# Performance work log

Hardware: AMD Instinct MI355X
Metric: run time of the kernel (lower is better)

## Reference

```python
import jax, jax.numpy as jnp
import numpy as np

N_NODES = 100000
N_EDGES = 3200000
NFEAT, NHID, NOUT = 256, 128, 64


def spmm(edge_row, edge_col, edge_val, dense):
    # out[r] = sum_{e: row[e]==r} val[e] * dense[col[e]]
    gathered = dense[edge_col] * edge_val[:, None]  # [E, F]
    return jax.ops.segment_sum(gathered, edge_row, num_segments=N_NODES)


def setup_inputs() -> dict:
    key = jax.random.key(0)
    ks = jax.random.split(key, 8)
    stdv1 = 1.0 / np.sqrt(NHID)
    stdv2 = 1.0 / np.sqrt(NOUT)
    return {
        "x": jax.random.normal(ks[0], (N_NODES, NFEAT), dtype=jnp.float32),
        "edge_row": jax.random.randint(ks[1], (N_EDGES,), 0, N_NODES, dtype=jnp.int32),
        "edge_col": jax.random.randint(ks[2], (N_EDGES,), 0, N_NODES, dtype=jnp.int32),
        "edge_val": jax.random.uniform(ks[3], (N_EDGES,), dtype=jnp.float32),
        "W1": jax.random.uniform(ks[4], (NFEAT, NHID), jnp.float32, -stdv1, stdv1),
        "b1": jax.random.uniform(ks[5], (NHID,), jnp.float32, -stdv1, stdv1),
        "W2": jax.random.uniform(ks[6], (NHID, NOUT), jnp.float32, -stdv2, stdv2),
        "b2": jax.random.uniform(ks[7], (NOUT,), jnp.float32, -stdv2, stdv2),
    }


def reference(x, edge_row, edge_col, edge_val, W1, b1, W2, b2):
    # layer 1: dense projection, SpMM aggregate, bias, ReLU
    support = x @ W1                                   # [N, NHID]
    h = spmm(edge_row, edge_col, edge_val, support) + b1
    h = jax.nn.relu(h)
    # dropout skipped (eval mode: training=False)
    # layer 2
    support2 = h @ W2                                  # [N, NOUT]
    out = spmm(edge_row, edge_col, edge_val, support2) + b2
    return out
```

## Files before the change

kernel.cpp:

```cpp
#include <hip/hip_runtime.h>
#include <hip/hip_bf16.h>

#define N_NODES 100000
#define N_EDGES 3200000
#define NFEAT 256
#define NHID 128
#define NOUT 64

#define BSHIFT 8
#define BROWS 256
#define NBUCK 391
#define EPB 4096
#define NBLK1 ((N_EDGES + EPB - 1) / EPB)

#define CSHIFT 12
#define NCLS 32

#define SM_SC    0
#define SM_SB    32768
#define SM_HIST  40960
#define SM_DELTA 42524
#define SM_SCANT 44088
#define SM_BYTES 44160

typedef __attribute__((ext_vector_type(8))) short short8;
typedef __attribute__((ext_vector_type(8))) unsigned short ushort8_t;
typedef __attribute__((ext_vector_type(4))) float f32x4;

__device__ __forceinline__ unsigned short f2bf(float f) {
    union { float f; unsigned int u; } v; v.f = f;
    unsigned int r = v.u + 0x7fffu + ((v.u >> 16) & 1u);
    return (unsigned short)(r >> 16);
}
__device__ __forceinline__ float bflo(unsigned int u) { return __uint_as_float(u << 16); }
__device__ __forceinline__ float bfhi(unsigned int u) { return __uint_as_float(u & 0xffff0000u); }


__global__ __launch_bounds__(256) void bcount_cvtw(const int* __restrict__ erow,
                                                   int* __restrict__ Mt,
                                                   const float* __restrict__ W1,
                                                   const float* __restrict__ W2,
                                                   unsigned short* __restrict__ W1b,
                                                   unsigned short* __restrict__ W2b) {
    __shared__ int h[NBUCK];
    if (blockIdx.x >= NBLK1) {
        const int i = (blockIdx.x - NBLK1) * 256 + threadIdx.x;
        if (i < NFEAT * NHID) W1b[i] = f2bf(W1[i]);
        if (i < NHID * NOUT)  W2b[i] = f2bf(W2[i]);
        return;
    }
    for (int i = threadIdx.x; i < NBUCK; i += 256) h[i] = 0;
    __syncthreads();
    const int base = blockIdx.x * EPB;
    const int n = min(EPB, N_EDGES - base);
    for (int i = threadIdx.x; i < n; i += 256)
        atomicAdd(&h[erow[base + i] >> BSHIFT], 1);
    __syncthreads();
    for (int b = threadIdx.x; b < NBUCK; b += 256)
        Mt[(size_t)b * NBLK1 + blockIdx.x] = h[b];
}


__global__ __launch_bounds__(256) void colscan_kernel(int* __restrict__ Mt,
                                                      int* __restrict__ btot) {
    const int wv = threadIdx.x >> 6, lane = threadIdx.x & 63;
    const int b = blockIdx.x * 4 + wv;
    if (b >= NBUCK) return;
    int* row = Mt + (size_t)b * NBLK1;
    int carry = 0;
    for (int t = 0; t < NBLK1; t += 64) {
        int i = t + lane;
        int v = (i < NBLK1) ? row[i] : 0;
        int x = v;
        #pragma unroll
        for (int off = 1; off < 64; off <<= 1) {
            int tt = __shfl_up(x, off);
            if (lane >= off) x += tt;
        }
        if (i < NBLK1) row[i] = carry + x - v;
        carry += __shfl(x, 63);
    }
    if (lane == 0) btot[b] = carry;
}


__global__ __launch_bounds__(1024) void bscan_kernel(const int* __restrict__ btot,
                                                     int* __restrict__ bbase) {
    __shared__ int wsum[16];
    const int tid = threadIdx.x;
    const int lane = tid & 63;
    int v = (tid < NBUCK) ? btot[tid] : 0;
    int x = v;
    #pragma unroll
    for (int off = 1; off < 64; off <<= 1) {
        int t = __shfl_up(x, off);
        if (lane >= off) x += t;
    }
    if (lane == 63) wsum[tid >> 6] = x;
    __syncthreads();
    if (tid < 16) {
        int s = wsum[tid];
        #pragma unroll
        for (int off = 1; off < 16; off <<= 1) {
            int t = __shfl_up(s, off);
            if (tid >= off) s += t;
        }
        wsum[tid] = s;
    }
    __syncthreads();
    if (tid >= 64) x += wsum[(tid >> 6) - 1];
    if (tid < NBUCK) bbase[tid] = x - v;
    if (tid == NBUCK - 1) bbase[NBUCK] = x;
}


__device__ __forceinline__ void binsort_role(int blk, char* sm,
                                             const int* __restrict__ erow,
                                             const int* __restrict__ ecol,
                                             const float* __restrict__ eval,
                                             const int* __restrict__ Mt,
                                             const int* __restrict__ btot,
                                             const int* __restrict__ bbase,
                                             int2* __restrict__ tmp) {
    int2* sc = (int2*)(sm + SM_SC);
    unsigned short* sb = (unsigned short*)(sm + SM_SB);
    int* hist  = (int*)(sm + SM_HIST);
    int* delta = (int*)(sm + SM_DELTA);
    int* scan_t = (int*)(sm + SM_SCANT);

    const int tid = threadIdx.x;
    const int base = blk * EPB;
    const int n = min(EPB, N_EDGES - base);

    int v0 = 0, v1 = 0, v2 = 0, v3 = 0;
    int m0 = 0, m1 = 0, m2 = 0, m3 = 0;
    {
        const int i0 = tid * 4;
        #define LOADCNT(k, vk, mk) { \
            int idx = i0 + k; \
            if (idx < NBUCK) { \
                mk = Mt[(size_t)idx * NBLK1 + blk]; \
                int nx = (blk + 1 < NBLK1) ? Mt[(size_t)idx * NBLK1 + blk + 1] : btot[idx]; \
                vk = nx - mk; \
            } }
        LOADCNT(0, v0, m0) LOADCNT(1, v1, m1) LOADCNT(2, v2, m2) LOADCNT(3, v3, m3)
        #undef LOADCNT
    }
    int s4 = v0 + v1 + v2 + v3;
    int xi = s4;
    const int lane = tid & 63;
    #pragma unroll
    for (int off = 1; off < 64; off <<= 1) {
        int t = __shfl_up(xi, off);
        if (lane >= off) xi += t;
    }
    if (lane == 63) scan_t[tid >> 6] = xi;
    __syncthreads();
    if (tid == 0) {
        int run = 0;
        #pragma unroll
        for (int w = 0; w < 4; ++w) { int t = scan_t[w]; scan_t[w] = run; run += t; }
    }
    __syncthreads();
    {
        int e0 = scan_t[tid >> 6] + xi - s4;
        int i0 = tid * 4;
        int ex[4] = {e0, e0 + v0, e0 + v0 + v1, e0 + v0 + v1 + v2};
        int mm[4] = {m0, m1, m2, m3};
        #pragma unroll
        for (int k = 0; k < 4; ++k) {
            int idx = i0 + k;
            if (idx < NBUCK) {
                hist[idx] = ex[k];
                delta[idx] = bbase[idx] + mm[k] - ex[k];
            }
        }
    }
    __syncthreads();

    for (int i = tid; i < n; i += 256) {
        int r = erow[base + i];
        int b = r >> BSHIFT;
        int rl = r & (BROWS - 1);
        int pos = atomicAdd(&hist[b], 1);
        sc[pos] = make_int2((rl << 17) | ecol[base + i], __float_as_int(eval[base + i]));
        sb[pos] = (unsigned short)b;
    }
    __syncthreads();

    for (int i = tid; i < n; i += 256) {
        int b = sb[i];
        tmp[delta[b] + i] = sc[i];
    }
}

__device__ __forceinline__ void gemm1_role(int bid, char* sm,
                                           const float* __restrict__ X,
                                           const unsigned short* __restrict__ Wb,
                                           unsigned short* __restrict__ Y) {
    unsigned short* bt = (unsigned short*)sm;
    const int tid = threadIdx.x;
    const int lane = tid & 63;
    const int w = tid >> 6;
    const int rb = bid * 128 + w * 32;
    const int lr = lane & 15;
    const int kg = lane >> 4;
    const int M = N_NODES;

    f32x4 acc[2][8];
    #pragma unroll
    for (int a = 0; a < 2; ++a)
        #pragma unroll
        for (int nf = 0; nf < 8; ++nf)
            #pragma unroll
            for (int i = 0; i < 4; ++i) acc[a][nf][i] = 0.f;

    for (int ph = 0; ph < 2; ++ph) {
        if (ph) __syncthreads();
        {
            const int nn = tid & 127;
            const int kb = tid >> 7;
            #pragma unroll
            for (int kk0 = 0; kk0 < 64; kk0 += 8) {
                const int kk = kb * 64 + kk0;
                unsigned short p[8];
                #pragma unroll
                for (int i = 0; i < 8; ++i)
                    p[i] = Wb[(size_t)(ph * 128 + kk + i) * NHID + nn];
                unsigned int byte = (unsigned int)nn * 256 + (unsigned int)kk * 2;
                byte ^= (unsigned int)(nn & 7) << 4;
                *(ushort8_t*)((char*)bt + byte) = *(const ushort8_t*)p;
            }
        }
        __syncthreads();

        #pragma unroll
        for (int ks = 0; ks < 4; ++ks) {
            const int k0 = ph * 128 + ks * 32 + kg * 8;
            short8 a0, a1;
            #pragma unroll
            for (int af = 0; af < 2; ++af) {
                const int row = rb + af * 16 + lr;
                short8 r;
                if (row < M) {
                    const float* p = X + (size_t)row * NFEAT + k0;
                    float4 u0 = *(const float4*)p;
                    float4 u1 = *(const float4*)(p + 4);
                    unsigned short q[8] = {f2bf(u0.x), f2bf(u0.y), f2bf(u0.z), f2bf(u0.w),
                                           f2bf(u1.x), f2bf(u1.y), f2bf(u1.z), f2bf(u1.w)};
                    r = *(const short8*)q;
                } else {
                    #pragma unroll
                    for (int i = 0; i < 8; ++i) r[i] = 0;
                }
                if (af == 0) a0 = r; else a1 = r;
            }
            #pragma unroll
            for (int nf = 0; nf < 8; ++nf) {
                const int nn = nf * 16 + lr;
                unsigned int byte = (unsigned int)nn * 256 + (unsigned int)(ks * 32 + kg * 8) * 2;
                byte ^= (unsigned int)(nn & 7) << 4;
                short8 bfr = *(const short8*)((const char*)bt + byte);
                acc[0][nf] = __builtin_amdgcn_mfma_f32_16x16x32_bf16(a0, bfr, acc[0][nf], 0, 0, 0);
                acc[1][nf] = __builtin_amdgcn_mfma_f32_16x16x32_bf16(a1, bfr, acc[1][nf], 0, 0, 0);
            }
        }
    }

    #pragma unroll
    for (int af = 0; af < 2; ++af)
        #pragma unroll
        for (int nf = 0; nf < 8; ++nf)
            #pragma unroll
            for (int i = 0; i < 4; ++i) {
                const int r = rb + af * 16 + kg * 4 + i;
                if (r < M) Y[(size_t)r * NHID + nf * 16 + lr] = f2bf(acc[af][nf][i]);
            }
}

__global__ __launch_bounds__(256) void fused_bg(const int* __restrict__ erow,
                                                const int* __restrict__ ecol,
                                                const float* __restrict__ eval,
                                                const int* __restrict__ Mt,
                                                const int* __restrict__ btot,
                                                const int* __restrict__ bbase,
                                                int2* __restrict__ tmp,
                                                const float* __restrict__ X,
                                                const unsigned short* __restrict__ W1b,
                                                unsigned short* __restrict__ Y) {
    extern __shared__ char sm[];
    const int idx = blockIdx.x >> 1;
    if (blockIdx.x & 1) gemm1_role(idx, sm, X, W1b, Y);
    else                binsort_role(idx, sm, erow, ecol, eval, Mt, btot, bbase, tmp);
}


__global__ __launch_bounds__(256) void rowsort_kernel(const int* __restrict__ bbase,
                                                      const int2* __restrict__ tmp,
                                                      int2* __restrict__ ec2,
                                                      int* __restrict__ rowptr) {
    __shared__ int h[BROWS * NCLS];
    __shared__ int wq[4];

    const int b = blockIdx.x;
    const int s = bbase[b], e = bbase[b + 1];
    const int n = e - s;
    const int tid = threadIdx.x;
    const int lane = tid & 63;

    for (int k = tid; k < BROWS * NCLS; k += 256) h[k] = 0;
    __syncthreads();

    for (int i = tid; i < n; i += 256) {
        unsigned int xx = (unsigned)tmp[s + i].x;
        unsigned int rl = xx >> 17;
        unsigned int c  = (xx & 0x1FFFFu) >> CSHIFT;
        atomicAdd(&h[(rl << 5) | ((c + rl) & 31)], 1);
    }
    __syncthreads();

    int tot = 0;
    #pragma unroll
    for (int j = 0; j < NCLS; ++j) tot += h[(tid << 5) | ((j + tid) & 31)];

    int x = tot;
    #pragma unroll
    for (int off = 1; off < 64; off <<= 1) {
        int t = __shfl_up(x, off);
        if (lane >= off) x += t;
    }
    if (lane == 63) wq[tid >> 6] = x;
    __syncthreads();
    if (tid == 0) {
        int run = 0;
        #pragma unroll
        for (int w = 0; w < 4; ++w) { int t = wq[w]; wq[w] = run; run += t; }
    }
    __syncthreads();
    x += wq[tid >> 6];
    {
        const int grow = b * BROWS + tid;
        if (grow < N_NODES) rowptr[grow + 1] = s + x;
        if (b == 0 && tid == 0) rowptr[0] = 0;
    }
    {
        int run = s + (x - tot);
        #pragma unroll
        for (int j = 0; j < NCLS; ++j) {
            const int idx = (tid << 5) | ((j + tid) & 31);
            const int cnt = h[idx];
            h[idx] = run;
            run += cnt;
        }
    }
    __syncthreads();

    for (int i = tid; i < n; i += 256) {
        int2 d = tmp[s + i];
        unsigned int xx = (unsigned)d.x;
        unsigned int rl = xx >> 17;
        unsigned int c  = (xx & 0x1FFFFu) >> CSHIFT;
        int pos = atomicAdd(&h[(rl << 5) | ((c + rl) & 31)], 1);
        ec2[pos] = make_int2(d.x & 0x1FFFF, d.y);
    }
}


template<int N, int K>
__global__ __launch_bounds__(256) void gemm_mfma(const unsigned short* __restrict__ X,
                                                 const unsigned short* __restrict__ Wb,
                                                 unsigned short* __restrict__ Y, int M) {
    __shared__ unsigned short bt[N * K];
    const int tid = threadIdx.x;

    {
        const int n = tid & (N - 1);
        const int kb = tid / N;
        const int kspan = K / (256 / N);
        for (int k0 = kb * kspan; k0 < (kb + 1) * kspan; k0 += 8) {
            unsigned short p[8];
            #pragma unroll
            for (int i = 0; i < 8; ++i) p[i] = Wb[(size_t)(k0 + i) * N + n];
            unsigned int byte = (unsigned int)n * (K * 2) + (unsigned int)k0 * 2;
            byte ^= (unsigned int)(n & 7) << 4;
            *(ushort8_t*)((char*)bt + byte) = *(const ushort8_t*)p;
        }
    }
    __syncthreads();

    const int lane = tid & 63;
    const int w = tid >> 6;
    const int rb = blockIdx.x * 128 + w * 32;
    const int lr = lane & 15;
    const int kg = lane >> 4;
    constexpr int NF = N / 16;
    constexpr int KS = K / 32;

    f32x4 acc[2][NF];
    #pragma unroll
    for (int a = 0; a < 2; ++a)
        #pragma unroll
        for (int nf = 0; nf < NF; ++nf)
            #pragma unroll
            for (int i = 0; i < 4; ++i) acc[a][nf][i] = 0.f;

    auto loadA = [&](int af, int ks) -> short8 {
        const int row = rb + af * 16 + lr;
        const int k0 = ks * 32 + kg * 8;
        short8 r;
        if (row < M) {
            r = *(const short8*)(X + (size_t)row * K + k0);
        } else {
            #pragma unroll
            for (int i = 0; i < 8; ++i) r[i] = 0;
        }
        return r;
    };
    auto loadB = [&](int nf, int ks) -> short8 {
        const int n = nf * 16 + lr;
        unsigned int byte = (unsigned int)n * (K * 2) + (unsigned int)(ks * 32 + kg * 8) * 2;
        byte ^= (unsigned int)(n & 7) << 4;
        return *(const short8*)((const char*)bt + byte);
    };

    #pragma unroll
    for (int ks = 0; ks < KS; ++ks) {
        short8 a0 = loadA(0, ks), a1 = loadA(1, ks);
        #pragma unroll
        for (int nf = 0; nf < NF; ++nf) {
            short8 bfr = loadB(nf, ks);
            acc[0][nf] = __builtin_amdgcn_mfma_f32_16x16x32_bf16(a0, bfr, acc[0][nf], 0, 0, 0);
            acc[1][nf] = __builtin_amdgcn_mfma_f32_16x16x32_bf16(a1, bfr, acc[1][nf], 0, 0, 0);
        }
    }

    #pragma unroll
    for (int af = 0; af < 2; ++af)
        #pragma unroll
        for (int nf = 0; nf < NF; ++nf)
            #pragma unroll
            for (int i = 0; i < 4; ++i) {
                const int r = rb + af * 16 + kg * 4 + i;
                if (r < M) Y[(size_t)r * N + nf * 16 + lr] = f2bf(acc[af][nf][i]);
            }
}


__global__ __launch_bounds__(256) void spmm1_kernel(const int* __restrict__ rp,
                                                    const int2* __restrict__ ec,
                                                    const unsigned int* __restrict__ d32,
                                                    const float* __restrict__ bias,
                                                    unsigned short* __restrict__ out) {
    const int lane = threadIdx.x & 63;
    const int row = blockIdx.x * 4 + (threadIdx.x >> 6);
    if (row >= N_NODES) return;
    const int s = __builtin_amdgcn_readfirstlane(rp[row]);
    const int e = __builtin_amdgcn_readfirstlane(rp[row + 1]);
    float a0 = 0.f, a1 = 0.f, b0 = 0.f, b1 = 0.f;
    float c0a = 0.f, c1a = 0.f, d0a = 0.f, d1a = 0.f;
    int j = s;
    for (; j + 16 <= e; j += 16) {
        int2 q0 = ec[j],      q1 = ec[j + 1],  q2 = ec[j + 2],  q3 = ec[j + 3];
        int2 q4 = ec[j + 4],  q5 = ec[j + 5],  q6 = ec[j + 6],  q7 = ec[j + 7];
        int2 q8 = ec[j + 8],  q9 = ec[j + 9],  qa = ec[j + 10], qb = ec[j + 11];
        int2 qc = ec[j + 12], qd = ec[j + 13], qe = ec[j + 14], qf = ec[j + 15];
        unsigned int u0 = d32[(size_t)q0.x * 64 + lane];
        unsigned int u1 = d32[(size_t)q1.x * 64 + lane];
        unsigned int u2 = d32[(size_t)q2.x * 64 + lane];
        unsigned int u3 = d32[(size_t)q3.x * 64 + lane];
        unsigned int u4 = d32[(size_t)q4.x * 64 + lane];
        unsigned int u5 = d32[(size_t)q5.x * 64 + lane];
        unsigned int u6 = d32[(size_t)q6.x * 64 + lane];
        unsigned int u7 = d32[(size_t)q7.x * 64 + lane];
        unsigned int u8 = d32[(size_t)q8.x * 64 + lane];
        unsigned int u9 = d32[(size_t)q9.x * 64 + lane];
        unsigned int ua = d32[(size_t)qa.x * 64 + lane];
        unsigned int ub = d32[(size_t)qb.x * 64 + lane];
        unsigned int uc = d32[(size_t)qc.x * 64 + lane];
        unsigned int ud = d32[(size_t)qd.x * 64 + lane];
        unsigned int ue = d32[(size_t)qe.x * 64 + lane];
        unsigned int uf = d32[(size_t)qf.x * 64 + lane];
        float v0 = __int_as_float(q0.y), v1 = __int_as_float(q1.y);
        float v2 = __int_as_float(q2.y), v3 = __int_as_float(q3.y);
        float v4 = __int_as_float(q4.y), v5 = __int_as_float(q5.y);
        float v6 = __int_as_float(q6.y), v7 = __int_as_float(q7.y);
        float v8 = __int_as_float(q8.y), v9 = __int_as_float(q9.y);
        float va = __int_as_float(qa.y), vb = __int_as_float(qb.y);
        float vc = __int_as_float(qc.y), vd = __int_as_float(qd.y);
        float ve = __int_as_float(qe.y), vf = __int_as_float(qf.y);
        a0 += v0 * bflo(u0); a1 += v0 * bfhi(u0);
        b0 += v1 * bflo(u1); b1 += v1 * bfhi(u1);
        c0a += v2 * bflo(u2); c1a += v2 * bfhi(u2);
        d0a += v3 * bflo(u3); d1a += v3 * bfhi(u3);
        a0 += v4 * bflo(u4); a1 += v4 * bfhi(u4);
        b0 += v5 * bflo(u5); b1 += v5 * bfhi(u5);
        c0a += v6 * bflo(u6); c1a += v6 * bfhi(u6);
        d0a += v7 * bflo(u7); d1a += v7 * bfhi(u7);
        a0 += v8 * bflo(u8); a1 += v8 * bfhi(u8);
        b0 += v9 * bflo(u9); b1 += v9 * bfhi(u9);
        c0a += va * bflo(ua); c1a += va * bfhi(ua);
        d0a += vb * bflo(ub); d1a += vb * bfhi(ub);
        a0 += vc * bflo(uc); a1 += vc * bfhi(uc);
        b0 += vd * bflo(ud); b1 += vd * bfhi(ud);
        c0a += ve * bflo(ue); c1a += ve * bfhi(ue);
        d0a += vf * bflo(uf); d1a += vf * bfhi(uf);
    }
    for (; j + 8 <= e; j += 8) {
        int2 q0 = ec[j],     q1 = ec[j + 1], q2 = ec[j + 2], q3 = ec[j + 3];
        int2 q4 = ec[j + 4], q5 = ec[j + 5], q6 = ec[j + 6], q7 = ec[j + 7];
        unsigned int u0 = d32[(size_t)q0.x * 64 + lane];
        unsigned int u1 = d32[(size_t)q1.x * 64 + lane];
        unsigned int u2 = d32[(size_t)q2.x * 64 + lane];
        unsigned int u3 = d32[(size_t)q3.x * 64 + lane];
        unsigned int u4 = d32[(size_t)q4.x * 64 + lane];
        unsigned int u5 = d32[(size_t)q5.x * 64 + lane];
        unsigned int u6 = d32[(size_t)q6.x * 64 + lane];
        unsigned int u7 = d32[(size_t)q7.x * 64 + lane];
        float v0 = __int_as_float(q0.y), v1 = __int_as_float(q1.y);
        float v2 = __int_as_float(q2.y), v3 = __int_as_float(q3.y);
        float v4 = __int_as_float(q4.y), v5 = __int_as_float(q5.y);
        float v6 = __int_as_float(q6.y), v7 = __int_as_float(q7.y);
        a0 += v0 * bflo(u0); a1 += v0 * bfhi(u0);
        b0 += v1 * bflo(u1); b1 += v1 * bfhi(u1);
        c0a += v2 * bflo(u2); c1a += v2 * bfhi(u2);
        d0a += v3 * bflo(u3); d1a += v3 * bfhi(u3);
        a0 += v4 * bflo(u4); a1 += v4 * bfhi(u4);
        b0 += v5 * bflo(u5); b1 += v5 * bfhi(u5);
        c0a += v6 * bflo(u6); c1a += v6 * bfhi(u6);
        d0a += v7 * bflo(u7); d1a += v7 * bfhi(u7);
    }
    for (; j < e; ++j) {
        int2 c = ec[j];
        float v = __int_as_float(c.y);
        unsigned int u = d32[(size_t)c.x * 64 + lane];
        a0 += v * bflo(u);
        a1 += v * bfhi(u);
    }
    a0 += b0 + c0a + d0a; a1 += b1 + c1a + d1a;
    float2 bp = *(const float2*)(bias + 2 * lane);
    float r0 = fmaxf(a0 + bp.x, 0.f);
    float r1 = fmaxf(a1 + bp.y, 0.f);
    unsigned int pack = (unsigned int)f2bf(r0) | ((unsigned int)f2bf(r1) << 16);
    *(unsigned int*)(out + (size_t)row * 128 + 2 * lane) = pack;
}


__global__ __launch_bounds__(256) void spmm2_kernel(const int* __restrict__ rp,
                                                    const int2* __restrict__ ec,
                                                    const unsigned int* __restrict__ d32,
                                                    const float* __restrict__ bias,
                                                    float* __restrict__ out) {
    const int lane = threadIdx.x & 63;
    const int row = blockIdx.x * 4 + (threadIdx.x >> 6);
    if (row >= N_NODES) return;
    const int s = __builtin_amdgcn_readfirstlane(rp[row]);
    const int e = __builtin_amdgcn_readfirstlane(rp[row + 1]);
    const int eh = lane >> 5, cl = lane & 31;
    float a0 = 0.f, a1 = 0.f, b0 = 0.f, b1 = 0.f;
    float c0a = 0.f, c1a = 0.f, d0a = 0.f, d1a = 0.f;
    int j = s;
    for (; j + 16 <= e; j += 16) {
        int2 q0 = ec[j + eh],      q1 = ec[j + 2 + eh];
        int2 q2 = ec[j + 4 + eh],  q3 = ec[j + 6 + eh];
        int2 q4 = ec[j + 8 + eh],  q5 = ec[j + 10 + eh];
        int2 q6 = ec[j + 12 + eh], q7 = ec[j + 14 + eh];
        unsigned int u0 = d32[(size_t)q0.x * 32 + cl];
        unsigned int u1 = d32[(size_t)q1.x * 32 + cl];
        unsigned int u2 = d32[(size_t)q2.x * 32 + cl];
        unsigned int u3 = d32[(size_t)q3.x * 32 + cl];
        unsigned int u4 = d32[(size_t)q4.x * 32 + cl];
        unsigned int u5 = d32[(size_t)q5.x * 32 + cl];
        unsigned int u6 = d32[(size_t)q6.x * 32 + cl];
        unsigned int u7 = d32[(size_t)q7.x * 32 + cl];
        float v0 = __int_as_float(q0.y), v1 = __int_as_float(q1.y);
        float v2 = __int_as_float(q2.y), v3 = __int_as_float(q3.y);
        float v4 = __int_as_float(q4.y), v5 = __int_as_float(q5.y);
        float v6 = __int_as_float(q6.y), v7 = __int_as_float(q7.y);
        a0 += v0 * bflo(u0); a1 += v0 * bfhi(u0);
        b0 += v1 * bflo(u1); b1 += v1 * bfhi(u1);
        c0a += v2 * bflo(u2); c1a += v2 * bfhi(u2);
        d0a += v3 * bflo(u3); d1a += v3 * bfhi(u3);
        a0 += v4 * bflo(u4); a1 += v4 * bfhi(u4);
        b0 += v5 * bflo(u5); b1 += v5 * bfhi(u5);
        c0a += v6 * bflo(u6); c1a += v6 * bfhi(u6);
        d0a += v7 * bflo(u7); d1a += v7 * bfhi(u7);
    }
    for (; j + 8 <= e; j += 8) {
        int2 q0 = ec[j + eh],     q1 = ec[j + 2 + eh];
        int2 q2 = ec[j + 4 + eh], q3 = ec[j + 6 + eh];
        unsigned int u0 = d32[(size_t)q0.x * 32 + cl];
        unsigned int u1 = d32[(size_t)q1.x * 32 + cl];
        unsigned int u2 = d32[(size_t)q2.x * 32 + cl];
        unsigned int u3 = d32[(size_t)q3.x * 32 + cl];
        float v0 = __int_as_float(q0.y), v1 = __int_as_float(q1.y);
        float v2 = __int_as_float(q2.y), v3 = __int_as_float(q3.y);
        a0 += v0 * bflo(u0); a1 += v0 * bfhi(u0);
        b0 += v1 * bflo(u1); b1 += v1 * bfhi(u1);
        c0a += v2 * bflo(u2); c1a += v2 * bfhi(u2);
        d0a += v3 * bflo(u3); d1a += v3 * bfhi(u3);
    }
    for (; j < e; j += 2) {
        const int j2 = j + eh;
        if (j2 < e) {
            int2 cv = ec[j2];
            float v = __int_as_float(cv.y);
            unsigned int u = d32[(size_t)cv.x * 32 + cl];
            a0 += v * bflo(u);
            a1 += v * bfhi(u);
        }
    }
    a0 += b0 + c0a + d0a; a1 += b1 + c1a + d1a;
    a0 += __shfl_xor(a0, 32);
    a1 += __shfl_xor(a1, 32);
    if (eh == 0) {
        float2 bp = *(const float2*)(bias + 2 * cl);
        *(float2*)(out + (size_t)row * 64 + 2 * cl) = make_float2(a0 + bp.x, a1 + bp.y);
    }
}


extern "C" void kernel_launch(void* const* d_in, const int* in_sizes, int n_in,
                              void* d_out, int out_size, void* d_ws, size_t ws_size,
                              hipStream_t stream) {
    const float* x    = (const float*)d_in[0];
    const int*   erow = (const int*)d_in[1];
    const int*   ecol = (const int*)d_in[2];
    const float* evalv = (const float*)d_in[3];
    const float* W1   = (const float*)d_in[4];
    const float* b1   = (const float*)d_in[5];
    const float* W2   = (const float*)d_in[6];
    const float* b2   = (const float*)d_in[7];
    float* out = (float*)d_out;

    char* wsp = (char*)d_ws;
    size_t off = 0;
    auto alloc = [&](size_t bytes) -> void* {
        void* p = wsp + off;
        off = (off + bytes + 255) & ~(size_t)255;
        return p;
    };
    unsigned short* support = (unsigned short*)alloc((size_t)N_NODES * NHID * 2);
    unsigned short* hbuf    = (unsigned short*)alloc((size_t)N_NODES * NHID * 2);
    int2*  tmp     = (int2*)alloc((size_t)N_EDGES * 8);
    int2*  ec2     = (int2*)alloc((size_t)N_EDGES * 8);
    int*   Mt      = (int*)alloc((size_t)NBUCK * NBLK1 * 4);
    int*   btot    = (int*)alloc((size_t)NBUCK * 4);
    int*   bbase   = (int*)alloc((size_t)(NBUCK + 1) * 4);
    int*   rowptr  = (int*)alloc((size_t)(N_NODES + 1) * 4);
    unsigned short* W1b = (unsigned short*)alloc((size_t)NFEAT * NHID * 2);
    unsigned short* W2b = (unsigned short*)alloc((size_t)NHID * NOUT * 2);

    bcount_cvtw<<<NBLK1 + 128, 256, 0, stream>>>(erow, Mt, W1, W2, W1b, W2b);
    colscan_kernel<<<(NBUCK + 3) / 4, 256, 0, stream>>>(Mt, btot);
    bscan_kernel<<<1, 1024, 0, stream>>>(btot, bbase);
    fused_bg<<<2 * NBLK1, 256, SM_BYTES, stream>>>(erow, ecol, evalv, Mt, btot, bbase,
                                                   tmp, x, W1b, support);
    rowsort_kernel<<<NBUCK, 256, 0, stream>>>(bbase, tmp, ec2, rowptr);

    spmm1_kernel<<<(N_NODES + 3) / 4, 256, 0, stream>>>(rowptr, ec2, (const unsigned int*)support, b1, hbuf);
    gemm_mfma<NOUT, NHID><<<(N_NODES + 127) / 128, 256, 0, stream>>>(hbuf, W2b, support, N_NODES);
    spmm2_kernel<<<(N_NODES + 3) / 4, 256, 0, stream>>>(rowptr, ec2, (const unsigned int*)support, b2, out);
}
```

Before: 331.3 us.

## Column-chunk SpMM traversal with multi-row waves for dense-row cache locality

Rowsort now emits per-row offsets for each of 13 column chunks (chunk width 8192 columns) in a new rowptr2 array. Both SpMM kernels give each wave 25 rows and walk all of them chunk by chunk, keeping 25 pairs of accumulators in registers. The aim is to keep the gathered dense rows within a small column band at any moment so they stay resident in L2. The cost is far fewer waves, very short inner loops per chunk (about two or three edges), heavy register use, and extra rowptr2 traffic, all of which can reduce the memory-level parallelism that a gather-bound kernel relies on.

```diff
diff --git a/kernel.cpp b/kernel.cpp
--- a/kernel.cpp
+++ b/kernel.cpp
@@ -13,8 +13,10 @@
 #define EPB 4096
 #define NBLK1 ((N_EDGES + EPB - 1) / EPB)
 
-#define CSHIFT 12
-#define NCLS 32
+#define CSHIFT 13
+#define NCLS 16
+#define NCHUNK 13
+#define RPW 25
 
 #define SM_SC    0
 #define SM_SB    32768
@@ -298,7 +300,8 @@
 __global__ __launch_bounds__(256) void rowsort_kernel(const int* __restrict__ bbase,
                                                       const int2* __restrict__ tmp,
                                                       int2* __restrict__ ec2,
-                                                      int* __restrict__ rowptr) {
+                                                      int* __restrict__ rowptr,
+                                                      int* __restrict__ rowptr2) {
     __shared__ int h[BROWS * NCLS];
     __shared__ int wq[4];
 
@@ -315,13 +318,13 @@
         unsigned int xx = (unsigned)tmp[s + i].x;
         unsigned int rl = xx >> 17;
         unsigned int c  = (xx & 0x1FFFFu) >> CSHIFT;
-        atomicAdd(&h[(rl << 5) | ((c + rl) & 31)], 1);
+        atomicAdd(&h[(rl << 4) | ((c + rl) & 15)], 1);
     }
     __syncthreads();
 
     int tot = 0;
     #pragma unroll
-    for (int j = 0; j < NCLS; ++j) tot += h[(tid << 5) | ((j + tid) & 31)];
+    for (int j = 0; j < NCLS; ++j) tot += h[(tid << 4) | ((j + tid) & 15)];
 
     int x = tot;
     #pragma unroll
@@ -338,18 +341,18 @@
     }
     __syncthreads();
     x += wq[tid >> 6];
-    {
-        const int grow = b * BROWS + tid;
-        if (grow < N_NODES) rowptr[grow + 1] = s + x;
-        if (b == 0 && tid == 0) rowptr[0] = 0;
-    }
+    const int grow = b * BROWS + tid;
+    if (grow < N_NODES) rowptr[grow + 1] = s + x;
+    if (b == 0 && tid == 0) rowptr[0] = 0;
+
     {
         int run = s + (x - tot);
         #pragma unroll
         for (int j = 0; j < NCLS; ++j) {
-            const int idx = (tid << 5) | ((j + tid) & 31);
+            const int idx = (tid << 4) | ((j + tid) & 15);
             const int cnt = h[idx];
             h[idx] = run;
+            if (grow < N_NODES) rowptr2[(size_t)grow * 16 + j] = run;
             run += cnt;
         }
     }
@@ -360,7 +363,7 @@
         unsigned int xx = (unsigned)d.x;
         unsigned int rl = xx >> 17;
         unsigned int c  = (xx & 0x1FFFFu) >> CSHIFT;
-        int pos = atomicAdd(&h[(rl << 5) | ((c + rl) & 31)], 1);
+        int pos = atomicAdd(&h[(rl << 4) | ((c + rl) & 15)], 1);
         ec2[pos] = make_int2(d.x & 0x1FFFF, d.y);
     }
 }
@@ -446,175 +449,120 @@
 }
 
 
-__global__ __launch_bounds__(256) void spmm1_kernel(const int* __restrict__ rp,
-                                                    const int2* __restrict__ ec,
-                                                    const unsigned int* __restrict__ d32,
-                                                    const float* __restrict__ bias,
-                                                    unsigned short* __restrict__ out) {
+__global__ __launch_bounds__(256, 4) void spmm1_kernel(const int* __restrict__ rp2,
+                                                       const int2* __restrict__ ec,
+                                                       const unsigned int* __restrict__ d32,
+                                                       const float* __restrict__ bias,
+                                                       unsigned short* __restrict__ out) {
     const int lane = threadIdx.x & 63;
-    const int row = blockIdx.x * 4 + (threadIdx.x >> 6);
-    if (row >= N_NODES) return;
-    const int s = __builtin_amdgcn_readfirstlane(rp[row]);
-    const int e = __builtin_amdgcn_readfirstlane(rp[row + 1]);
-    float a0 = 0.f, a1 = 0.f, b0 = 0.f, b1 = 0.f;
-    float c0a = 0.f, c1a = 0.f, d0a = 0.f, d1a = 0.f;
-    int j = s;
-    for (; j + 16 <= e; j += 16) {
-        int2 q0 = ec[j],      q1 = ec[j + 1],  q2 = ec[j + 2],  q3 = ec[j + 3];
-        int2 q4 = ec[j + 4],  q5 = ec[j + 5],  q6 = ec[j + 6],  q7 = ec[j + 7];
-        int2 q8 = ec[j + 8],  q9 = ec[j + 9],  qa = ec[j + 10], qb = ec[j + 11];
-        int2 qc = ec[j + 12], qd = ec[j + 13], qe = ec[j + 14], qf = ec[j + 15];
-        unsigned int u0 = d32[(size_t)q0.x * 64 + lane];
-        unsigned int u1 = d32[(size_t)q1.x * 64 + lane];
-        unsigned int u2 = d32[(size_t)q2.x * 64 + lane];
-        unsigned int u3 = d32[(size_t)q3.x * 64 + lane];
-        unsigned int u4 = d32[(size_t)q4.x * 64 + lane];
-        unsigned int u5 = d32[(size_t)q5.x * 64 + lane];
-        unsigned int u6 = d32[(size_t)q6.x * 64 + lane];
-        unsigned int u7 = d32[(size_t)q7.x * 64 + lane];
-        unsigned int u8 = d32[(size_t)q8.x * 64 + lane];
-        unsigned int u9 = d32[(size_t)q9.x * 64 + lane];
-        unsigned int ua = d32[(size_t)qa.x * 64 + lane];
-        unsigned int ub = d32[(size_t)qb.x * 64 + lane];
-        unsigned int uc = d32[(size_t)qc.x * 64 + lane];
-        unsigned int ud = d32[(size_t)qd.x * 64 + lane];
-        unsigned int ue = d32[(size_t)qe.x * 64 + lane];
-        unsigned int uf = d32[(size_t)qf.x * 64 + lane];
-        float v0 = __int_as_float(q0.y), v1 = __int_as_float(q1.y);
-        float v2 = __int_as_float(q2.y), v3 = __int_as_float(q3.y);
-        float v4 = __int_as_float(q4.y), v5 = __int_as_float(q5.y);
-        float v6 = __int_as_float(q6.y), v7 = __int_as_float(q7.y);
-        float v8 = __int_as_float(q8.y), v9 = __int_as_float(q9.y);
-        float va = __int_as_float(qa.y), vb = __int_as_float(qb.y);
-        float vc = __int_as_float(qc.y), vd = __int_as_float(qd.y);
-        float ve = __int_as_float(qe.y), vf = __int_as_float(qf.y);
-        a0 += v0 * bflo(u0); a1 += v0 * bfhi(u0);
-        b0 += v1 * bflo(u1); b1 += v1 * bfhi(u1);
-        c0a += v2 * bflo(u2); c1a += v2 * bfhi(u2);
-        d0a += v3 * bflo(u3); d1a += v3 * bfhi(u3);
-        a0 += v4 * bflo(u4); a1 += v4 * bfhi(u4);
-        b0 += v5 * bflo(u5); b1 += v5 * bfhi(u5);
-        c0a += v6 * bflo(u6); c1a += v6 * bfhi(u6);
-        d0a += v7 * bflo(u7); d1a += v7 * bfhi(u7);
-        a0 += v8 * bflo(u8); a1 += v8 * bfhi(u8);
-        b0 += v9 * bflo(u9); b1 += v9 * bfhi(u9);
-        c0a += va * bflo(ua); c1a += va * bfhi(ua);
-        d0a += vb * bflo(ub); d1a += vb * bfhi(ub);
-        a0 += vc * bflo(uc); a1 += vc * bfhi(uc);
-        b0 += vd * bflo(ud); b1 += vd * bfhi(ud);
-        c0a += ve * bflo(ue); c1a += ve * bfhi(ue);
-        d0a += vf * bflo(uf); d1a += vf * bfhi(uf);
-    }
-    for (; j + 8 <= e; j += 8) {
-        int2 q0 = ec[j],     q1 = ec[j + 1], q2 = ec[j + 2], q3 = ec[j + 3];
-        int2 q4 = ec[j + 4], q5 = ec[j + 5], q6 = ec[j + 6], q7 = ec[j + 7];
-        unsigned int u0 = d32[(size_t)q0.x * 64 + lane];
-        unsigned int u1 = d32[(size_t)q1.x * 64 + lane];
-        unsigned int u2 = d32[(size_t)q2.x * 64 + lane];
-        unsigned int u3 = d32[(size_t)q3.x * 64 + lane];
-        unsigned int u4 = d32[(size_t)q4.x * 64 + lane];
-        unsigned int u5 = d32[(size_t)q5.x * 64 + lane];
-        unsigned int u6 = d32[(size_t)q6.x * 64 + lane];
-        unsigned int u7 = d32[(size_t)q7.x * 64 + lane];
-        float v0 = __int_as_float(q0.y), v1 = __int_as_float(q1.y);
-        float v2 = __int_as_float(q2.y), v3 = __int_as_float(q3.y);
-        float v4 = __int_as_float(q4.y), v5 = __int_as_float(q5.y);
-        float v6 = __int_as_float(q6.y), v7 = __int_as_float(q7.y);
-        a0 += v0 * bflo(u0); a1 += v0 * bfhi(u0);
-        b0 += v1 * bflo(u1); b1 += v1 * bfhi(u1);
-        c0a += v2 * bflo(u2); c1a += v2 * bfhi(u2);
-        d0a += v3 * bflo(u3); d1a += v3 * bfhi(u3);
-        a0 += v4 * bflo(u4); a1 += v4 * bfhi(u4);
-        b0 += v5 * bflo(u5); b1 += v5 * bfhi(u5);
-        c0a += v6 * bflo(u6); c1a += v6 * bfhi(u6);
-        d0a += v7 * bflo(u7); d1a += v7 * bfhi(u7);
-    }
-    for (; j < e; ++j) {
-        int2 c = ec[j];
-        float v = __int_as_float(c.y);
-        unsigned int u = d32[(size_t)c.x * 64 + lane];
-        a0 += v * bflo(u);
-        a1 += v * bfhi(u);
-    }
-    a0 += b0 + c0a + d0a; a1 += b1 + c1a + d1a;
-    float2 bp = *(const float2*)(bias + 2 * lane);
-    float r0 = fmaxf(a0 + bp.x, 0.f);
-    float r1 = fmaxf(a1 + bp.y, 0.f);
-    unsigned int pack = (unsigned int)f2bf(r0) | ((unsigned int)f2bf(r1) << 16);
-    *(unsigned int*)(out + (size_t)row * 128 + 2 * lane) = pack;
-}
-
-
-__global__ __launch_bounds__(256) void spmm2_kernel(const int* __restrict__ rp,
-                                                    const int2* __restrict__ ec,
-                                                    const unsigned int* __restrict__ d32,
-                                                    const float* __restrict__ bias,
-                                                    float* __restrict__ out) {
+    const int wv = threadIdx.x >> 6;
+    const int row0 = blockIdx.x * (4 * RPW) + wv * RPW;
+
+    float aL[RPW], aH[RPW];
+    #pragma unroll
+    for (int r = 0; r < RPW; ++r) { aL[r] = 0.f; aH[r] = 0.f; }
+
+    for (int k = 0; k < NCHUNK; ++k) {
+        #pragma unroll
+        for (int r = 0; r < RPW; ++r) {
+            const int row = row0 + r;
+            const int s = __builtin_amdgcn_readfirstlane(rp2[(size_t)row * 16 + k]);
+            const int e = __builtin_amdgcn_readfirstlane(rp2[(size_t)row * 16 + k + 1]);
+            int j = s;
+            for (; j + 4 <= e; j += 4) {
+                int2 q0 = ec[j], q1 = ec[j + 1], q2 = ec[j + 2], q3 = ec[j + 3];
+                unsigned int u0 = d32[(size_t)q0.x * 64 + lane];
+                unsigned int u1 = d32[(size_t)q1.x * 64 + lane];
+                unsigned int u2 = d32[(size_t)q2.x * 64 + lane];
+                unsigned int u3 = d32[(size_t)q3.x * 64 + lane];
+                float v0 = __int_as_float(q0.y), v1 = __int_as_float(q1.y);
+                float v2 = __int_as_float(q2.y), v3 = __int_as_float(q3.y);
+                aL[r] += v0 * bflo(u0); aH[r] += v0 * bfhi(u0);
+                aL[r] += v1 * bflo(u1); aH[r] += v1 * bfhi(u1);
+                aL[r] += v2 * bflo(u2); aH[r] += v2 * bfhi(u2);
+                aL[r] += v3 * bflo(u3); aH[r] += v3 * bfhi(u3);
+            }
+            if (j + 2 <= e) {
+                int2 q0 = ec[j], q1 = ec[j + 1];
+                unsigned int u0 = d32[(size_t)q0.x * 64 + lane];
+                unsigned int u1 = d32[(size_t)q1.x * 64 + lane];
+                float v0 = __int_as_float(q0.y), v1 = __int_as_float(q1.y);
+                aL[r] += v0 * bflo(u0); aH[r] += v0 * bfhi(u0);
+                aL[r] += v1 * bflo(u1); aH[r] += v1 * bfhi(u1);
+                j += 2;
+            }
+            if (j < e) {
+                int2 q0 = ec[j];
+                unsigned int u0 = d32[(size_t)q0.x * 64 + lane];
+                float v0 = __int_as_float(q0.y);
+                aL[r] += v0 * bflo(u0); aH[r] += v0 * bfhi(u0);
+            }
+        }
+    }
+
+    const float2 bp = *(const float2*)(bias + 2 * lane);
+    #pragma unroll
+    for (int r = 0; r < RPW; ++r) {
+        const int row = row0 + r;
+        float r0 = fmaxf(aL[r] + bp.x, 0.f);
+        float r1 = fmaxf(aH[r] + bp.y, 0.f);
+        unsigned int pack = (unsigned int)f2bf(r0) | ((unsigned int)f2bf(r1) << 16);
+        *(unsigned int*)(out + (size_t)row * 128 + 2 * lane) = pack;
+    }
+}
+
+
+__global__ __launch_bounds__(256, 4) void spmm2_kernel(const int* __restrict__ rp2,
+                                                       const int2* __restrict__ ec,
+                                                       const unsigned int* __restrict__ d32,
+                                                       const float* __restrict__ bias,
+                                                       float* __restrict__ out) {
     const int lane = threadIdx.x & 63;
-    const int row = blockIdx.x * 4 + (threadIdx.x >> 6);
-    if (row >= N_NODES) return;
-    const int s = __builtin_amdgcn_readfirstlane(rp[row]);
-    const int e = __builtin_amdgcn_readfirstlane(rp[row + 1]);
+    const int wv = threadIdx.x >> 6;
+    const int row0 = blockIdx.x * (4 * RPW) + wv * RPW;
     const int eh = lane >> 5, cl = lane & 31;
-    float a0 = 0.f, a1 = 0.f, b0 = 0.f, b1 = 0.f;
-    float c0a = 0.f, c1a = 0.f, d0a = 0.f, d1a = 0.f;
-    int j = s;
-    for (; j + 16 <= e; j += 16) {
-        int2 q0 = ec[j + eh],      q1 = ec[j + 2 + eh];
-        int2 q2 = ec[j + 4 + eh],  q3 = ec[j + 6 + eh];
-        int2 q4 = ec[j + 8 + eh],  q5 = ec[j + 10 + eh];
-        int2 q6 = ec[j + 12 + eh], q7 = ec[j + 14 + eh];
-        unsigned int u0 = d32[(size_t)q0.x * 32 + cl];
-        unsigned int u1 = d32[(size_t)q1.x * 32 + cl];
-        unsigned int u2 = d32[(size_t)q2.x * 32 + cl];
-        unsigned int u3 = d32[(size_t)q3.x * 32 + cl];
-        unsigned int u4 = d32[(size_t)q4.x * 32 + cl];
-        unsigned int u5 = d32[(size_t)q5.x * 32 + cl];
-        unsigned int u6 = d32[(size_t)q6.x * 32 + cl];
-        unsigned int u7 = d32[(size_t)q7.x * 32 + cl];
-        float v0 = __int_as_float(q0.y), v1 = __int_as_float(q1.y);
-        float v2 = __int_as_float(q2.y), v3 = __int_as_float(q3.y);
-        float v4 = __int_as_float(q4.y), v5 = __int_as_float(q5.y);
-        float v6 = __int_as_float(q6.y), v7 = __int_as_float(q7.y);
-        a0 += v0 * bflo(u0); a1 += v0 * bfhi(u0);
-        b0 += v1 * bflo(u1); b1 += v1 * bfhi(u1);
-        c0a += v2 * bflo(u2); c1a += v2 * bfhi(u2);
-        d0a += v3 * bflo(u3); d1a += v3 * bfhi(u3);
-        a0 += v4 * bflo(u4); a1 += v4 * bfhi(u4);
-        b0 += v5 * bflo(u5); b1 += v5 * bfhi(u5);
-        c0a += v6 * bflo(u6); c1a += v6 * bfhi(u6);
-        d0a += v7 * bflo(u7); d1a += v7 * bfhi(u7);
-    }
-    for (; j + 8 <= e; j += 8) {
-        int2 q0 = ec[j + eh],     q1 = ec[j + 2 + eh];
-        int2 q2 = ec[j + 4 + eh], q3 = ec[j + 6 + eh];
-        unsigned int u0 = d32[(size_t)q0.x * 32 + cl];
-        unsigned int u1 = d32[(size_t)q1.x * 32 + cl];
-        unsigned int u2 = d32[(size_t)q2.x * 32 + cl];
-        unsigned int u3 = d32[(size_t)q3.x * 32 + cl];
-        float v0 = __int_as_float(q0.y), v1 = __int_as_float(q1.y);
-        float v2 = __int_as_float(q2.y), v3 = __int_as_float(q3.y);
-        a0 += v0 * bflo(u0); a1 += v0 * bfhi(u0);
-        b0 += v1 * bflo(u1); b1 += v1 * bfhi(u1);
-        c0a += v2 * bflo(u2); c1a += v2 * bfhi(u2);
-        d0a += v3 * bflo(u3); d1a += v3 * bfhi(u3);
-    }
-    for (; j < e; j += 2) {
-        const int j2 = j + eh;
-        if (j2 < e) {
-            int2 cv = ec[j2];
-            float v = __int_as_float(cv.y);
-            unsigned int u = d32[(size_t)cv.x * 32 + cl];
-            a0 += v * bflo(u);
-            a1 += v * bfhi(u);
-        }
-    }
-    a0 += b0 + c0a + d0a; a1 += b1 + c1a + d1a;
-    a0 += __shfl_xor(a0, 32);
-    a1 += __shfl_xor(a1, 32);
-    if (eh == 0) {
-        float2 bp = *(const float2*)(bias + 2 * cl);
-        *(float2*)(out + (size_t)row * 64 + 2 * cl) = make_float2(a0 + bp.x, a1 + bp.y);
+
+    float aL[RPW], aH[RPW];
+    #pragma unroll
+    for (int r = 0; r < RPW; ++r) { aL[r] = 0.f; aH[r] = 0.f; }
+
+    for (int k = 0; k < NCHUNK; ++k) {
+        #pragma unroll
+        for (int r = 0; r < RPW; ++r) {
+            const int row = row0 + r;
+            const int s = __builtin_amdgcn_readfirstlane(rp2[(size_t)row * 16 + k]);
+            const int e = __builtin_amdgcn_readfirstlane(rp2[(size_t)row * 16 + k + 1]);
+            int j = s;
+            for (; j + 4 <= e; j += 4) {
+                int2 q0 = ec[j + eh], q1 = ec[j + 2 + eh];
+                unsigned int u0 = d32[(size_t)q0.x * 32 + cl];
+                unsigned int u1 = d32[(size_t)q1.x * 32 + cl];
+                float v0 = __int_as_float(q0.y), v1 = __int_as_float(q1.y);
+                aL[r] += v0 * bflo(u0); aH[r] += v0 * bfhi(u0);
+                aL[r] += v1 * bflo(u1); aH[r] += v1 * bfhi(u1);
+            }
+            while (j < e) {
+                const int j2 = j + eh;
+                if (j2 < e) {
+                    int2 q0 = ec[j2];
+                    unsigned int u0 = d32[(size_t)q0.x * 32 + cl];
+                    float v0 = __int_as_float(q0.y);
+                    aL[r] += v0 * bflo(u0); aH[r] += v0 * bfhi(u0);
+                }
+                j += 2;
+            }
+        }
+    }
+
+    const float2 bp = *(const float2*)(bias + 2 * cl);
+    #pragma unroll
+    for (int r = 0; r < RPW; ++r) {
+        const int row = row0 + r;
+        float a0 = aL[r] + __shfl_xor(aL[r], 32);
+        float a1 = aH[r] + __shfl_xor(aH[r], 32);
+        if (eh == 0) {
+            *(float2*)(out + (size_t)row * 64 + 2 * cl) = make_float2(a0 + bp.x, a1 + bp.y);
+        }
     }
 }
 
@@ -647,6 +595,7 @@
     int*   btot    = (int*)alloc((size_t)NBUCK * 4);
     int*   bbase   = (int*)alloc((size_t)(NBUCK + 1) * 4);
     int*   rowptr  = (int*)alloc((size_t)(N_NODES + 1) * 4);
+    int*   rowptr2 = (int*)alloc((size_t)N_NODES * 16 * 4);
     unsigned short* W1b = (unsigned short*)alloc((size_t)NFEAT * NHID * 2);
     unsigned short* W2b = (unsigned short*)alloc((size_t)NHID * NOUT * 2);
 
@@ -655,9 +604,9 @@
     bscan_kernel<<<1, 1024, 0, stream>>>(btot, bbase);
     fused_bg<<<2 * NBLK1, 256, SM_BYTES, stream>>>(erow, ecol, evalv, Mt, btot, bbase,
                                                    tmp, x, W1b, support);
-    rowsort_kernel<<<NBUCK, 256, 0, stream>>>(bbase, tmp, ec2, rowptr);
-
-    spmm1_kernel<<<(N_NODES + 3) / 4, 256, 0, stream>>>(rowptr, ec2, (const unsigned int*)support, b1, hbuf);
+    rowsort_kernel<<<NBUCK, 256, 0, stream>>>(bbase, tmp, ec2, rowptr, rowptr2);
+
+    spmm1_kernel<<<N_NODES / (4 * RPW), 256, 0, stream>>>(rowptr2, ec2, (const unsigned int*)support, b1, hbuf);
     gemm_mfma<NOUT, NHID><<<(N_NODES + 127) / 128, 256, 0, stream>>>(hbuf, W2b, support, N_NODES);
-    spmm2_kernel<<<(N_NODES + 3) / 4, 256, 0, stream>>>(rowptr, ec2, (const unsigned int*)support, b2, out);
-}
+    spmm2_kernel<<<N_NODES / (4 * RPW), 256, 0, stream>>>(rowptr2, ec2, (const unsigned int*)support, b2, out);
+}
```

Result: slower. 828.0 us (+149.9%).
